# Kernel tuning notes

Measured on AMD Instinct MI355X. Metric: run time of the kernel, lower is better.

## Reference

```python
import jax, jax.numpy as jnp
import numpy as np

N, M, F = 16384, 16384, 512
NUM_BATCHES = 16


def setup_inputs() -> dict:
    key = jax.random.key(0)
    k1, k2, k3, k4 = jax.random.split(key, 4)
    H_q = jax.random.normal(k1, (N, F), dtype=jnp.float32)
    H_c = jax.random.normal(k2, (M, F), dtype=jnp.float32)
    batch_q = jnp.sort(jax.random.randint(k3, (N,), 0, NUM_BATCHES, dtype=jnp.int64))
    batch_c = jnp.sort(jax.random.randint(k4, (M,), 0, NUM_BATCHES, dtype=jnp.int64))
    return {"H_q": H_q, "H_c": H_c, "batch_q": batch_q, "batch_c": batch_c}


def reference(H_q, H_c, batch_q, batch_c):
    # scores: [n, m] dense dot-product similarity
    scores = jnp.matmul(H_q, H_c.T)
    # mask[i, j] = True iff query i and candidate j belong to the same batch element
    mask = batch_q[:, None] == batch_c[None, :]
    out = jnp.where(mask, scores, -jnp.inf)
    return out, mask
```

## Files before the change

### kernel.cpp

```cpp
#include <hip/hip_runtime.h>
#include <hip/hip_bf16.h>
#include <math.h>


#define BM 128
#define BN 128
#define NEG_BIG (-3.3895313892515355e+38f)

typedef float    f32x4  __attribute__((ext_vector_type(4)));
typedef unsigned u32x4  __attribute__((ext_vector_type(4)));
typedef short    short8 __attribute__((ext_vector_type(8)));

__device__ __forceinline__ void st_nt(float* p, f32x4 v) {
    __builtin_nontemporal_store(v, (f32x4*)p);
}
__device__ __forceinline__ void st_nt1(float* p, float v) {
    __builtin_nontemporal_store(v, p);
}

__device__ __forceinline__ unsigned pk2(float a, float b) {
    unsigned ua = __builtin_bit_cast(unsigned, a);
    unsigned ub = __builtin_bit_cast(unsigned, b);
    return (ub & 0xFFFF0000u) | (ua >> 16);
}

__global__ __launch_bounds__(256) void dot_tile_kernel(
    const float* __restrict__ Hq, const float* __restrict__ Hc,
    const int* __restrict__ bq, const int* __restrict__ bc,
    float* __restrict__ out, float* __restrict__ mask_out,
    int M, int F, int ntx, int write_mask)
{
    const int t = threadIdx.x;

    int bid = blockIdx.x;
    const int nwg = gridDim.x;
    if ((nwg & 7) == 0) {
        const int q = nwg >> 3;
        bid = (bid & 7) * q + (bid >> 3);
    }

    const int i0 = (bid / ntx) * BM;
    const int j0 = (bid % ntx) * BN;

    if (!(bq[i0] <= bc[j0 + BN - 1] && bc[j0] <= bq[i0 + BM - 1])) {
        const f32x4 m4 = (f32x4){NEG_BIG, NEG_BIG, NEG_BIG, NEG_BIG};
        const f32x4 z4 = (f32x4){0.f, 0.f, 0.f, 0.f};
        #pragma unroll
        for (int v = 0; v < 16; ++v) {
            const int idx = t + v * 256;
            const int r   = idx >> 5;
            const int c4  = idx & 31;
            const size_t off = (size_t)(i0 + r) * M + j0 + c4 * 4;
            st_nt(out + off, m4);
            if (write_mask) st_nt(mask_out + off, z4);
        }
        return;
    }

    __shared__ short Abf[128 * 32];
    __shared__ short Bbf[128 * 32];
    __shared__ int bql[BM];
    __shared__ int bcl[BN];

    if (t < BM) bql[t] = bq[i0 + t];
    else        bcl[t - BM] = bc[j0 + (t - BM)];

    f32x4 acc[4][4];
    #pragma unroll
    for (int a = 0; a < 4; ++a)
        #pragma unroll
        for (int b = 0; b < 4; ++b) acc[a][b] = (f32x4){0.f, 0.f, 0.f, 0.f};

    const int l   = t & 63;
    const int wid = t >> 6;
    const int wr  = wid >> 1;
    const int wc  = wid & 1;
    const int lg  = l >> 4;
    const int lm  = l & 15;

    const int sr   = t >> 1;
    const int half = t & 1;
    const int swW = ((sr >> 1) & 3) << 4;
    const int wb0 = sr * 64 + half * 32;
    const int swR = ((lm >> 1) & 3) << 4;

    char* Ab = (char*)Abf;
    char* Bb = (char*)Bbf;

    const int nks = F >> 5;

    const float* aptrf = Hq + (size_t)(i0 + sr) * F + half * 16;
    const float* bptrf = Hc + (size_t)(j0 + sr) * F + half * 16;

    for (int ks = 0; ks < nks; ++ks) {
        const int k0 = ks * 32;
        f32x4 a0 = *(const f32x4*)(aptrf + k0);
        f32x4 a1 = *(const f32x4*)(aptrf + k0 + 4);
        f32x4 a2 = *(const f32x4*)(aptrf + k0 + 8);
        f32x4 a3 = *(const f32x4*)(aptrf + k0 + 12);
        f32x4 b0 = *(const f32x4*)(bptrf + k0);
        f32x4 b1 = *(const f32x4*)(bptrf + k0 + 4);
        f32x4 b2 = *(const f32x4*)(bptrf + k0 + 8);
        f32x4 b3 = *(const f32x4*)(bptrf + k0 + 12);
        u32x4 pa0 = (u32x4){pk2(a0[0],a0[1]), pk2(a0[2],a0[3]), pk2(a1[0],a1[1]), pk2(a1[2],a1[3])};
        u32x4 pa1 = (u32x4){pk2(a2[0],a2[1]), pk2(a2[2],a2[3]), pk2(a3[0],a3[1]), pk2(a3[2],a3[3])};
        u32x4 pb0 = (u32x4){pk2(b0[0],b0[1]), pk2(b0[2],b0[3]), pk2(b1[0],b1[1]), pk2(b1[2],b1[3])};
        u32x4 pb1 = (u32x4){pk2(b2[0],b2[1]), pk2(b2[2],b2[3]), pk2(b3[0],b3[1]), pk2(b3[2],b3[3])};
        __syncthreads();
        *(u32x4*)(Ab + ((wb0     ) ^ swW)) = pa0;
        *(u32x4*)(Ab + ((wb0 + 16) ^ swW)) = pa1;
        *(u32x4*)(Bb + ((wb0     ) ^ swW)) = pb0;
        *(u32x4*)(Bb + ((wb0 + 16) ^ swW)) = pb1;
        __syncthreads();
        short8 af[4], bf[4];
        #pragma unroll
        for (int m = 0; m < 4; ++m) {
            const int arow = wr * 64 + m * 16 + lm;
            af[m] = *(const short8*)(Ab + arow * 64 + ((lg * 16) ^ swR));
            const int brow = wc * 64 + m * 16 + lm;
            bf[m] = *(const short8*)(Bb + brow * 64 + ((lg * 16) ^ swR));
        }
        #pragma unroll
        for (int m = 0; m < 4; ++m)
            #pragma unroll
            for (int n = 0; n < 4; ++n)
                acc[m][n] = __builtin_amdgcn_mfma_f32_16x16x32_bf16(
                    af[m], bf[n], acc[m][n], 0, 0, 0);
    }

    #pragma unroll
    for (int m = 0; m < 4; ++m) {
        #pragma unroll
        for (int v = 0; v < 4; ++v) {
            const int rit = wr * 64 + m * 16 + lg * 4 + v;
            const int bqv = bql[rit];
            const size_t rowoff = (size_t)(i0 + rit) * M + j0;
            #pragma unroll
            for (int n = 0; n < 4; ++n) {
                const int cit = wc * 64 + n * 16 + lm;
                const bool eq = (bqv == bcl[cit]);
                st_nt1(out + rowoff + cit, eq ? acc[m][n][v] : NEG_BIG);
                if (write_mask) st_nt1(mask_out + rowoff + cit, eq ? 1.0f : 0.0f);
            }
        }
    }
}

extern "C" void kernel_launch(void* const* d_in, const int* in_sizes, int n_in,
                              void* d_out, int out_size, void* d_ws, size_t ws_size,
                              hipStream_t stream) {
    const float* Hq = (const float*)d_in[0];
    const float* Hc = (const float*)d_in[1];
    const int*   bq = (const int*)d_in[2];
    const int*   bc = (const int*)d_in[3];

    const int N = in_sizes[2];
    const int M = in_sizes[3];
    const int F = in_sizes[0] / N;

    float* out = (float*)d_out;
    const long long NM = (long long)N * M;
    const int write_mask = ((long long)out_size >= 2 * NM) ? 1 : 0;
    float* mask_out = out + NM;

    const int nty = N / BM;
    const int ntx = M / BN;

    dot_tile_kernel<<<nty * ntx, 256, 0, stream>>>(
        Hq, Hc, bq, bc, out, mask_out, M, F, ntx, write_mask);
}
```

Baseline: 417.2 us.

## Reshape output tile to 64x256 with four waves splitting columns

The block tile changes from 128x128 to 64x256. All four waves now share the same 64 query rows and each wave owns a 64-column slice. The global-to-LDS load mapping is rewritten so each thread loads one A chunk and four B chunks per k-step. The aim is a finer row granularity for the batch-overlap skip test and wider contiguous row segments in the stores. In exchange, each tile loads more total operand data, A 64 rows plus B 256 rows against 256 before, and the skip/compute tile boundaries shift.

```diff
diff --git a/kernel.cpp b/kernel.cpp
--- a/kernel.cpp
+++ b/kernel.cpp
@@ -3,8 +3,8 @@
 #include <math.h>
 
 
-#define BM 128
-#define BN 128
+#define BM 64
+#define BN 256
 #define NEG_BIG (-3.3895313892515355e+38f)
 
 typedef float    f32x4  __attribute__((ext_vector_type(4)));
@@ -48,8 +48,8 @@
         #pragma unroll
         for (int v = 0; v < 16; ++v) {
             const int idx = t + v * 256;
-            const int r   = idx >> 5;
-            const int c4  = idx & 31;
+            const int r   = idx >> 6;
+            const int c4  = idx & 63;
             const size_t off = (size_t)(i0 + r) * M + j0 + c4 * 4;
             st_nt(out + off, m4);
             if (write_mask) st_nt(mask_out + off, z4);
@@ -57,13 +57,13 @@
         return;
     }
 
-    __shared__ short Abf[128 * 32];
-    __shared__ short Bbf[128 * 32];
+    __shared__ short Abf[64 * 32];
+    __shared__ short Bbf[256 * 32];
     __shared__ int bql[BM];
     __shared__ int bcl[BN];
 
     if (t < BM) bql[t] = bq[i0 + t];
-    else        bcl[t - BM] = bc[j0 + (t - BM)];
+    bcl[t] = bc[j0 + t];
 
     f32x4 acc[4][4];
     #pragma unroll
@@ -73,15 +73,9 @@
 
     const int l   = t & 63;
     const int wid = t >> 6;
-    const int wr  = wid >> 1;
-    const int wc  = wid & 1;
     const int lg  = l >> 4;
     const int lm  = l & 15;
 
-    const int sr   = t >> 1;
-    const int half = t & 1;
-    const int swW = ((sr >> 1) & 3) << 4;
-    const int wb0 = sr * 64 + half * 32;
     const int swR = ((lm >> 1) & 3) << 4;
 
     char* Ab = (char*)Abf;
@@ -89,35 +83,36 @@
 
     const int nks = F >> 5;
 
-    const float* aptrf = Hq + (size_t)(i0 + sr) * F + half * 16;
-    const float* bptrf = Hc + (size_t)(j0 + sr) * F + half * 16;
-
     for (int ks = 0; ks < nks; ++ks) {
-        const int k0 = ks * 32;
-        f32x4 a0 = *(const f32x4*)(aptrf + k0);
-        f32x4 a1 = *(const f32x4*)(aptrf + k0 + 4);
-        f32x4 a2 = *(const f32x4*)(aptrf + k0 + 8);
-        f32x4 a3 = *(const f32x4*)(aptrf + k0 + 12);
-        f32x4 b0 = *(const f32x4*)(bptrf + k0);
-        f32x4 b1 = *(const f32x4*)(bptrf + k0 + 4);
-        f32x4 b2 = *(const f32x4*)(bptrf + k0 + 8);
-        f32x4 b3 = *(const f32x4*)(bptrf + k0 + 12);
-        u32x4 pa0 = (u32x4){pk2(a0[0],a0[1]), pk2(a0[2],a0[3]), pk2(a1[0],a1[1]), pk2(a1[2],a1[3])};
-        u32x4 pa1 = (u32x4){pk2(a2[0],a2[1]), pk2(a2[2],a2[3]), pk2(a3[0],a3[1]), pk2(a3[2],a3[3])};
-        u32x4 pb0 = (u32x4){pk2(b0[0],b0[1]), pk2(b0[2],b0[3]), pk2(b1[0],b1[1]), pk2(b1[2],b1[3])};
-        u32x4 pb1 = (u32x4){pk2(b2[0],b2[1]), pk2(b2[2],b2[3]), pk2(b3[0],b3[1]), pk2(b3[2],b3[3])};
+        const int kf = ks * 32;
+        u32x4 pk[5];
+        int   off[5];
+        #pragma unroll
+        for (int j = 0; j < 5; ++j) {
+            const int c  = t + 256 * j;
+            const bool isA = (j == 0);
+            const int cc = isA ? c : c - 256;
+            const int row = cc >> 2;
+            const int qq  = cc & 3;
+            const float* src = isA ? (Hq + (size_t)(i0 + row) * F + kf + qq * 8)
+                                   : (Hc + (size_t)(j0 + row) * F + kf + qq * 8);
+            f32x4 x0 = *(const f32x4*)(src);
+            f32x4 x1 = *(const f32x4*)(src + 4);
+            pk[j] = (u32x4){pk2(x0[0],x0[1]), pk2(x0[2],x0[3]),
+                            pk2(x1[0],x1[1]), pk2(x1[2],x1[3])};
+            off[j] = (row * 64 + qq * 16) ^ (((row >> 1) & 3) << 4);
+        }
         __syncthreads();
-        *(u32x4*)(Ab + ((wb0     ) ^ swW)) = pa0;
-        *(u32x4*)(Ab + ((wb0 + 16) ^ swW)) = pa1;
-        *(u32x4*)(Bb + ((wb0     ) ^ swW)) = pb0;
-        *(u32x4*)(Bb + ((wb0 + 16) ^ swW)) = pb1;
+        *(u32x4*)(Ab + off[0]) = pk[0];
+        #pragma unroll
+        for (int j = 1; j < 5; ++j) *(u32x4*)(Bb + off[j]) = pk[j];
         __syncthreads();
         short8 af[4], bf[4];
         #pragma unroll
         for (int m = 0; m < 4; ++m) {
-            const int arow = wr * 64 + m * 16 + lm;
+            const int arow = m * 16 + lm;
             af[m] = *(const short8*)(Ab + arow * 64 + ((lg * 16) ^ swR));
-            const int brow = wc * 64 + m * 16 + lm;
+            const int brow = wid * 64 + m * 16 + lm;
             bf[m] = *(const short8*)(Bb + brow * 64 + ((lg * 16) ^ swR));
         }
         #pragma unroll
@@ -132,12 +127,12 @@
     for (int m = 0; m < 4; ++m) {
         #pragma unroll
         for (int v = 0; v < 4; ++v) {
-            const int rit = wr * 64 + m * 16 + lg * 4 + v;
+            const int rit = m * 16 + lg * 4 + v;
             const int bqv = bql[rit];
             const size_t rowoff = (size_t)(i0 + rit) * M + j0;
             #pragma unroll
             for (int n = 0; n < 4; ++n) {
-                const int cit = wc * 64 + n * 16 + lm;
+                const int cit = wid * 64 + n * 16 + lm;
                 const bool eq = (bqv == bcl[cit]);
                 st_nt1(out + rowoff + cit, eq ? acc[m][n][v] : NEG_BIG);
                 if (write_mask) st_nt1(mask_out + rowoff + cit, eq ? 1.0f : 0.0f);
```

New measurement: 391.0 us. -6.3%, faster.
